# Performance work log

Hardware: AMD Instinct MI355X
Metric: run time of the kernel (lower is better)

Reference implementation:

```python
import jax, jax.numpy as jnp
import numpy as np

ALPHA = 1.0
EPS = 1e-7


def _giou_loss(pred, tgt):
    # pred, tgt: [..., 4] in (x1, y1, x2, y2); returns per-box loss 1 - GIoU
    px1, py1, px2, py2 = pred[..., 0], pred[..., 1], pred[..., 2], pred[..., 3]
    tx1, ty1, tx2, ty2 = tgt[..., 0], tgt[..., 1], tgt[..., 2], tgt[..., 3]
    area_p = (px2 - px1) * (py2 - py1)
    area_t = (tx2 - tx1) * (ty2 - ty1)
    iw = jnp.clip(jnp.minimum(px2, tx2) - jnp.maximum(px1, tx1), 0.0)
    ih = jnp.clip(jnp.minimum(py2, ty2) - jnp.maximum(py1, ty1), 0.0)
    inter = iw * ih
    union = area_p + area_t - inter
    iou = inter / (union + EPS)
    cw = jnp.maximum(px2, tx2) - jnp.minimum(px1, tx1)
    ch = jnp.maximum(py2, ty2) - jnp.minimum(py1, ty1)
    area_c = cw * ch
    giou = iou - (area_c - union) / (area_c + EPS)
    return 1.0 - giou


def _make_boxes(key, shape):
    k1, k2 = jax.random.split(key)
    xy1 = jax.random.uniform(k1, shape + (2,), jnp.float32) * 0.5
    wh = jax.random.uniform(k2, shape + (2,), jnp.float32) * 0.4 + 0.01
    return jnp.concatenate([xy1, xy1 + wh], axis=-1)


def setup_inputs() -> dict:
    key = jax.random.key(0)
    kc, kl, kt, kcls, kp = jax.random.split(key, 5)
    B, A, C = 64, 8732, 81
    confidences = jax.random.normal(kc, (B, A, C), jnp.float32)
    localizations = _make_boxes(kl, (B, A))
    tboxes = _make_boxes(kt, (B, A))
    is_pos = jax.random.uniform(kp, (B, A)) < 0.02
    cls = jnp.where(is_pos, jax.random.randint(kcls, (B, A), 1, C), 0)
    targets = jnp.concatenate([tboxes, cls[..., None].astype(jnp.float32)], axis=-1)
    return {"confidences": confidences, "localizations": localizations, "targets": targets}


def reference(confidences, localizations, targets):
    B, A, C = confidences.shape
    labels = targets[..., 4].astype(jnp.int32)     # [B, A]
    tboxes = targets[..., :4]                      # [B, A, 4]
    pos = labels > 0                               # [B, A]
    nm = pos.sum(axis=-1)                          # [B] num matched per item

    logp = jax.nn.log_softmax(confidences, axis=-1)          # [B, A, C]
    ce = -jnp.take_along_axis(logp, labels[..., None], axis=-1)[..., 0]  # CE vs label
    pos_loss = jnp.where(pos, ce, 0.0).sum(axis=-1)          # [B]

    # hard negative mining: CE vs background (class 0) on negatives only,
    # sort descending, keep top 3 * num_matched. CE >= 0, so mark positives
    # with -1 sentinel; they sort to the end and are excluded by (>= 0).
    neg_ce = jnp.where(pos, -1.0, -logp[..., 0])             # [B, A]
    sneg = -jnp.sort(-neg_ce, axis=-1)                       # descending
    ranks = jnp.arange(A)
    take = (ranks[None, :] < (3 * nm)[:, None]) & (sneg >= 0.0)
    neg_loss = jnp.where(take, sneg, 0.0).sum(axis=-1)       # [B]

    gl = _giou_loss(localizations, tboxes)                   # [B, A]
    loc_loss = jnp.where(pos, gl, 0.0).sum(axis=-1)          # [B]

    num_hits = nm.sum()
    total = (pos_loss + neg_loss + ALPHA * loc_loss).sum()
    denom = jnp.maximum(num_hits, 1).astype(total.dtype)
    has_hits = num_hits > 0
    loss = jnp.where(has_hits, total / denom, 0.0)
    conf_breakdown = jnp.where(has_hits, (pos_loss + neg_loss).sum() / denom, 0.0)
    loc_breakdown = jnp.where(has_hits, loc_loss.sum() / denom, 0.0)
    return loss, conf_breakdown, loc_breakdown
```

## Files before the change

### kernel.cpp

```cpp
#include <hip/hip_runtime.h>
#include <math.h>

#define NCLS 81
#define A_ANCH 8732
#define B_BATCH 64
#define NANCH (B_BATCH * A_ANCH)
#define EPSF 1e-7f

#define TILE 32
#define TDW  (TILE * NCLS)
#define BUFDW 2624
#define NT (NANCH / TILE)
#define GRID1 1792

static const size_t SBYTES = (size_t)NANCH * sizeof(float);

__global__ __launch_bounds__(64) void lse_kernel(
    const float* __restrict__ conf, float* __restrict__ sout,
    double* __restrict__ accum, unsigned long long* __restrict__ hits,
    unsigned int* __restrict__ done)
{
    __shared__ float sb[2][BUFDW];

    int tid = threadIdx.x;
    if (blockIdx.x == 0 && tid == 0) {
        accum[0] = 0.0; accum[1] = 0.0; *hits = 0ull; *done = 0u;
    }

    int a = tid & 31, h = tid >> 5;
    int t = blockIdx.x;

    float4 q0, q1, q2, q3, q4, q5, q6, q7, q8, q9;
    float qt = 0.f;

    {
        const float4* p = (const float4*)conf + (size_t)t * (TDW / 4);
        q0 = p[0 * 64 + tid]; q1 = p[1 * 64 + tid]; q2 = p[2 * 64 + tid];
        q3 = p[3 * 64 + tid]; q4 = p[4 * 64 + tid]; q5 = p[5 * 64 + tid];
        q6 = p[6 * 64 + tid]; q7 = p[7 * 64 + tid]; q8 = p[8 * 64 + tid];
        q9 = p[9 * 64 + tid];
        if (tid < 32) qt = conf[(size_t)t * TDW + 2560 + tid];
        float4* lp = (float4*)&sb[0][0];
        lp[0 * 64 + tid] = q0; lp[1 * 64 + tid] = q1; lp[2 * 64 + tid] = q2;
        lp[3 * 64 + tid] = q3; lp[4 * 64 + tid] = q4; lp[5 * 64 + tid] = q5;
        lp[6 * 64 + tid] = q6; lp[7 * 64 + tid] = q7; lp[8 * 64 + tid] = q8;
        lp[9 * 64 + tid] = q9;
        if (tid < 32) sb[0][2560 + tid] = qt;
    }
    int par = 0;

    #pragma clang loop unroll(disable)
    while (true) {
        int tn = t + GRID1;
        bool more = (tn < NT);
        if (more) {
            const float4* p = (const float4*)conf + (size_t)tn * (TDW / 4);
            q0 = p[0 * 64 + tid]; q1 = p[1 * 64 + tid]; q2 = p[2 * 64 + tid];
            q3 = p[3 * 64 + tid]; q4 = p[4 * 64 + tid]; q5 = p[5 * 64 + tid];
            q6 = p[6 * 64 + tid]; q7 = p[7 * 64 + tid]; q8 = p[8 * 64 + tid];
            q9 = p[9 * 64 + tid];
            if (tid < 32) qt = conf[(size_t)tn * TDW + 2560 + tid];
        }

        const float* r = &sb[par][a * 81 + h * 40];
        float x0 = r[0];
        float s0 = 0.f, s1 = 0.f, s2 = 0.f, s3 = 0.f;
        #pragma unroll
        for (int j = 0; j < 40; j += 4) {
            s0 += __expf(r[j]);
            s1 += __expf(r[j + 1]);
            s2 += __expf(r[j + 2]);
            s3 += __expf(r[j + 3]);
        }
        float s = (s0 + s1) + (s2 + s3) + (float)h * __expf(r[40]);
        s += __shfl_xor(s, 32);
        float res = __logf(s) - x0;

        if (!more) {
            if (h == 0) sout[(size_t)t * TILE + a] = res;
            break;
        }

        {
            float4* lp = (float4*)&sb[par ^ 1][0];
            lp[0 * 64 + tid] = q0; lp[1 * 64 + tid] = q1; lp[2 * 64 + tid] = q2;
            lp[3 * 64 + tid] = q3; lp[4 * 64 + tid] = q4; lp[5 * 64 + tid] = q5;
            lp[6 * 64 + tid] = q6; lp[7 * 64 + tid] = q7; lp[8 * 64 + tid] = q8;
            lp[9 * 64 + tid] = q9;
            if (tid < 32) sb[par ^ 1][2560 + tid] = qt;
        }
        if (h == 0) sout[(size_t)t * TILE + a] = res;

        t = tn; par ^= 1;
    }
}

#define K2_T 1024
#define VPT 9
#define NBIN 4096

__global__ __launch_bounds__(K2_T) void mine_kernel(
    const float* __restrict__ conf, const float* __restrict__ loc,
    const float* __restrict__ tgt, const float* __restrict__ sout,
    double* __restrict__ accum, unsigned long long* __restrict__ hits,
    unsigned int* __restrict__ done, float* __restrict__ out)
{
    __shared__ int   hist[NBIN];
    __shared__ int   wsum[16];
    __shared__ int   wex[16];
    __shared__ int   selB, selCab;
    __shared__ float fs[4];
    __shared__ int   c0_s, cg_s, nm_s;

    int b = blockIdx.x, tid = threadIdx.x;
    int lane = tid & 63, wid = tid >> 6;

    for (int i = tid; i < NBIN; i += K2_T) hist[i] = 0;
    if (tid < 4)  fs[tid] = 0.f;
    if (tid == 0) { c0_s = 0; cg_s = 0; nm_s = 0; }
    __syncthreads();

    float v[VPT]; int lab[VPT];
    size_t base = (size_t)b * A_ANCH;
    #pragma unroll
    for (int i = 0; i < VPT; ++i) {
        int idx = tid + i * K2_T;
        bool in = idx < A_ANCH;
        v[i]   = in ? sout[base + idx] : -1.f;
        lab[i] = in ? (int)tgt[(base + idx) * 5 + 4] : 0;
    }

    float pce = 0.f, ploc = 0.f; int pc = 0;
    #pragma unroll
    for (int i = 0; i < VPT; ++i) {
        if (lab[i] > 0) {
            size_t gi = base + (size_t)(tid + i * K2_T);
            float r0 = conf[gi * NCLS];
            float rl = conf[gi * NCLS + lab[i]];
            pce += v[i] + r0 - rl;
            float4 p = *(const float4*)(loc + gi * 4);
            const float* tg = tgt + gi * 5;
            float tx1 = tg[0], ty1 = tg[1], tx2 = tg[2], ty2 = tg[3];
            float area_p = (p.z - p.x) * (p.w - p.y);
            float area_t = (tx2 - tx1) * (ty2 - ty1);
            float iw = fmaxf(fminf(p.z, tx2) - fmaxf(p.x, tx1), 0.f);
            float ih = fmaxf(fminf(p.w, ty2) - fmaxf(p.y, ty1), 0.f);
            float inter = iw * ih;
            float uni   = area_p + area_t - inter;
            float iou   = inter / (uni + EPSF);
            float cw = fmaxf(p.z, tx2) - fminf(p.x, tx1);
            float ch = fmaxf(p.w, ty2) - fminf(p.y, ty1);
            float area_c = cw * ch;
            ploc += 1.f - (iou - (area_c - uni) / (area_c + EPSF));
            pc++;
            v[i] = -1.f;
        }
    }
    int c = 0; float sa = 0.f;
    #pragma unroll
    for (int i = 0; i < VPT; ++i) { if (v[i] >= 0.f) { c++; sa += v[i]; } }
    for (int off = 32; off; off >>= 1) {
        pc += __shfl_xor(pc, off);  pce += __shfl_xor(pce, off);
        ploc += __shfl_xor(ploc, off);
        c  += __shfl_xor(c, off);   sa  += __shfl_xor(sa, off);
    }
    if (lane == 0) {
        if (pc) atomicAdd(&nm_s, pc);
        atomicAdd(&fs[2], pce);
        atomicAdd(&fs[3], ploc);
        atomicAdd(&c0_s, c);
        atomicAdd(&fs[0], sa);
    }
    __syncthreads();

    int k = 3 * nm_s;
    int c0 = c0_s; float sall = fs[0];
    float negl = 0.f;

    if (k > 0) {
        if (k >= c0) {
            negl = sall;
        } else {
            int B1v = 0, B2v = 0, kk = k;
            for (int lvl = 0; lvl < 2; ++lvl) {
                if (lvl == 1) {
                    for (int i = tid; i < NBIN; i += K2_T) hist[i] = 0;
                    __syncthreads();
                }
                #pragma unroll
                for (int i = 0; i < VPT; ++i) {
                    if (v[i] >= 0.f) {
                        unsigned bits = __float_as_uint(v[i]);
                        if (lvl == 0) {
                            atomicAdd(&hist[bits >> 19], 1);
                        } else if ((int)(bits >> 19) == B1v) {
                            atomicAdd(&hist[(bits >> 7) & 4095], 1);
                        }
                    }
                }
                __syncthreads();

                int b0 = tid * 4;
                int h0 = hist[b0], h1 = hist[b0 + 1], h2 = hist[b0 + 2], h3 = hist[b0 + 3];
                int tsum = h0 + h1 + h2 + h3;
                int ssum = tsum;
                #pragma unroll
                for (int off = 1; off < 64; off <<= 1) {
                    int o = __shfl_down(ssum, off);
                    ssum += (lane + off < 64) ? o : 0;
                }
                if (lane == 0) wsum[wid] = ssum;
                __syncthreads();
                if (wid == 0) {
                    int wv = (lane < 16) ? wsum[lane] : 0;
                    int ws = wv;
                    #pragma unroll
                    for (int off = 1; off < 64; off <<= 1) {
                        int o = __shfl_down(ws, off);
                        ws += (lane + off < 64) ? o : 0;
                    }
                    if (lane < 16) wex[lane] = ws - wv;
                }
                __syncthreads();
                int above = wex[wid] + (ssum - tsum);
                if (above < kk && above + tsum >= kk) {
                    int cum = above, B = b0;
                    if      (cum + h3 >= kk) { B = b0 + 3; }
                    else if (cum + h3 + h2 >= kk) { cum += h3; B = b0 + 2; }
                    else if (cum + h3 + h2 + h1 >= kk) { cum += h3 + h2; B = b0 + 1; }
                    else { cum += h3 + h2 + h1; B = b0; }
                    selB = B; selCab = cum;
                }
                __syncthreads();
                if (lvl == 0) { B1v = selB; } else { B2v = selB; }
                kk -= selCab;
                __syncthreads();
            }

            unsigned tk = ((unsigned)B1v << 12) | (unsigned)B2v;
            float tval = __uint_as_float(((unsigned)B1v << 19) | ((unsigned)B2v << 7));
            int cg = 0; float sg = 0.f;
            #pragma unroll
            for (int i = 0; i < VPT; ++i) {
                if (v[i] >= 0.f) {
                    unsigned key = __float_as_uint(v[i]) >> 7;
                    if (key > tk) { cg++; sg += v[i]; }
                }
            }
            for (int off = 32; off; off >>= 1) {
                cg += __shfl_xor(cg, off); sg += __shfl_xor(sg, off);
            }
            if (lane == 0) { atomicAdd(&cg_s, cg); atomicAdd(&fs[1], sg); }
            __syncthreads();
            negl = fs[1] + (float)(k - cg_s) * tval;
        }
    }

    if (tid == 0) {
        atomicAdd(&accum[0], (double)(fs[2] + negl));
        atomicAdd(&accum[1], (double)fs[3]);
        atomicAdd(hits, (unsigned long long)nm_s);
        __threadfence();
        unsigned old = atomicAdd(done, 1u);
        if (old == B_BATCH - 1) {
            double conf_s = __hip_atomic_load(&accum[0], __ATOMIC_ACQUIRE, __HIP_MEMORY_SCOPE_AGENT);
            double loc_s  = __hip_atomic_load(&accum[1], __ATOMIC_ACQUIRE, __HIP_MEMORY_SCOPE_AGENT);
            unsigned long long h = __hip_atomic_load(hits, __ATOMIC_ACQUIRE, __HIP_MEMORY_SCOPE_AGENT);
            double denom = (double)(h > 0 ? h : 1ull);
            if (h > 0) {
                out[0] = (float)((conf_s + loc_s) / denom);
                out[1] = (float)(conf_s / denom);
                out[2] = (float)(loc_s / denom);
            } else {
                out[0] = 0.f; out[1] = 0.f; out[2] = 0.f;
            }
        }
    }
}

extern "C" void kernel_launch(void* const* d_in, const int* in_sizes, int n_in,
                              void* d_out, int out_size, void* d_ws, size_t ws_size,
                              hipStream_t stream) {
    const float* conf = (const float*)d_in[0];
    const float* loc  = (const float*)d_in[1];
    const float* tgt  = (const float*)d_in[2];
    float* out = (float*)d_out;

    char* ws = (char*)d_ws;
    float* sout = (float*)ws;
    double* accum = (double*)(ws + SBYTES);
    unsigned long long* hits = (unsigned long long*)(ws + SBYTES + 16);
    unsigned int* done = (unsigned int*)(ws + SBYTES + 24);

    lse_kernel<<<dim3(GRID1), dim3(64), 0, stream>>>(conf, sout, accum, hits, done);
    mine_kernel<<<dim3(B_BATCH), dim3(K2_T), 0, stream>>>(
        conf, loc, tgt, sout, accum, hits, done, out);
}
```

Before: 50.18 us.

## Compute per-anchor logsumexp from registers without shared-memory staging

The LSE kernel drops the double-buffered shared-memory tile and instead has each group of 8 lanes load float4 pieces of 4 anchors' rows straight from global memory. Each lane accumulates exponentials into per-anchor partial sums, using compile-time boundary handling for float4s that straddle two rows, then reduces with xor shuffles. The aim is to remove the LDS write/read traffic and barriers, and to raise occupancy with 256-thread blocks and more waves. The cost is the loss of the explicit load/compute overlap across tiles, plus extra select logic and shuffles in each group.

```diff
diff --git a/kernel.cpp b/kernel.cpp
--- a/kernel.cpp
+++ b/kernel.cpp
@@ -7,91 +7,78 @@
 #define NANCH (B_BATCH * A_ANCH)
 #define EPSF 1e-7f
 
-#define TILE 32
-#define TDW  (TILE * NCLS)
-#define BUFDW 2624
-#define NT (NANCH / TILE)
-#define GRID1 1792
+#define GROUPS (NANCH / 32)
+#define LBLK 256
+#define LGRID 2183
+#define NWAVE (LGRID * 4)
 
 static const size_t SBYTES = (size_t)NANCH * sizeof(float);
 
-__global__ __launch_bounds__(64) void lse_kernel(
+#define ACC_ADD(KK, val) do {            \
+    if      ((KK) == 0) a0 += (val);     \
+    else if ((KK) == 1) a1 += (val);     \
+    else if ((KK) == 2) a2 += (val);     \
+    else                a3 += (val);     \
+} while (0)
+
+#define PROC(r, c, comp) do {                              \
+    const int lo = 32 * (r) + (c);                         \
+    const int K  = lo / 81;                                \
+    const int K2 = (lo + 28) / 81;                         \
+    float ev = __expf(comp);                               \
+    if (K == K2) { ACC_ADD(K, ev); }                       \
+    else {                                                 \
+        const int T = (81 * (K + 1) - lo + 3) / 4;         \
+        float hv = (j >= T) ? ev : 0.f;                    \
+        ACC_ADD(K, ev - hv); ACC_ADD(K + 1, hv);           \
+    }                                                      \
+} while (0)
+
+#define PROCQ(r, qv) do {        \
+    PROC(r, 0, (qv).x);          \
+    PROC(r, 1, (qv).y);          \
+    PROC(r, 2, (qv).z);          \
+    PROC(r, 3, (qv).w);          \
+} while (0)
+
+__global__ __launch_bounds__(LBLK) void lse_kernel(
     const float* __restrict__ conf, float* __restrict__ sout,
     double* __restrict__ accum, unsigned long long* __restrict__ hits,
     unsigned int* __restrict__ done)
 {
-    __shared__ float sb[2][BUFDW];
-
     int tid = threadIdx.x;
     if (blockIdx.x == 0 && tid == 0) {
         accum[0] = 0.0; accum[1] = 0.0; *hits = 0ull; *done = 0u;
     }
-
-    int a = tid & 31, h = tid >> 5;
-    int t = blockIdx.x;
-
-    float4 q0, q1, q2, q3, q4, q5, q6, q7, q8, q9;
-    float qt = 0.f;
-
-    {
-        const float4* p = (const float4*)conf + (size_t)t * (TDW / 4);
-        q0 = p[0 * 64 + tid]; q1 = p[1 * 64 + tid]; q2 = p[2 * 64 + tid];
-        q3 = p[3 * 64 + tid]; q4 = p[4 * 64 + tid]; q5 = p[5 * 64 + tid];
-        q6 = p[6 * 64 + tid]; q7 = p[7 * 64 + tid]; q8 = p[8 * 64 + tid];
-        q9 = p[9 * 64 + tid];
-        if (tid < 32) qt = conf[(size_t)t * TDW + 2560 + tid];
-        float4* lp = (float4*)&sb[0][0];
-        lp[0 * 64 + tid] = q0; lp[1 * 64 + tid] = q1; lp[2 * 64 + tid] = q2;
-        lp[3 * 64 + tid] = q3; lp[4 * 64 + tid] = q4; lp[5 * 64 + tid] = q5;
-        lp[6 * 64 + tid] = q6; lp[7 * 64 + tid] = q7; lp[8 * 64 + tid] = q8;
-        lp[9 * 64 + tid] = q9;
-        if (tid < 32) sb[0][2560 + tid] = qt;
-    }
-    int par = 0;
+    int w = blockIdx.x * 4 + (tid >> 6);
+    int lane = tid & 63;
+    int o = lane >> 3, j = lane & 7;
 
     #pragma clang loop unroll(disable)
-    while (true) {
-        int tn = t + GRID1;
-        bool more = (tn < NT);
-        if (more) {
-            const float4* p = (const float4*)conf + (size_t)tn * (TDW / 4);
-            q0 = p[0 * 64 + tid]; q1 = p[1 * 64 + tid]; q2 = p[2 * 64 + tid];
-            q3 = p[3 * 64 + tid]; q4 = p[4 * 64 + tid]; q5 = p[5 * 64 + tid];
-            q6 = p[6 * 64 + tid]; q7 = p[7 * 64 + tid]; q8 = p[8 * 64 + tid];
-            q9 = p[9 * 64 + tid];
-            if (tid < 32) qt = conf[(size_t)tn * TDW + 2560 + tid];
-        }
-
-        const float* r = &sb[par][a * 81 + h * 40];
-        float x0 = r[0];
-        float s0 = 0.f, s1 = 0.f, s2 = 0.f, s3 = 0.f;
+    for (int g = w; g < GROUPS; g += NWAVE) {
+        const float4* p = (const float4*)conf + (size_t)g * 648 + o * 81 + j;
+        float4 q0 = p[0],  q1 = p[8],  q2 = p[16], q3 = p[24], q4 = p[32];
+        float4 q5 = p[40], q6 = p[48], q7 = p[56], q8 = p[64], q9 = p[72];
+        float4 q10 = make_float4(-INFINITY, -INFINITY, -INFINITY, -INFINITY);
+        if (j == 0) q10 = p[80];
+        float x0 = 0.f;
+        if (j < 4) x0 = conf[(size_t)g * 2592 + (o * 4 + j) * 81];
+
+        float a0 = 0.f, a1 = 0.f, a2 = 0.f, a3 = 0.f;
+        PROCQ(0, q0); PROCQ(1, q1); PROCQ(2, q2); PROCQ(3, q3); PROCQ(4, q4);
+        PROCQ(5, q5); PROCQ(6, q6); PROCQ(7, q7); PROCQ(8, q8); PROCQ(9, q9);
+        a3 += __expf(q10.x); a3 += __expf(q10.y);
+        a3 += __expf(q10.z); a3 += __expf(q10.w);
+
         #pragma unroll
-        for (int j = 0; j < 40; j += 4) {
-            s0 += __expf(r[j]);
-            s1 += __expf(r[j + 1]);
-            s2 += __expf(r[j + 2]);
-            s3 += __expf(r[j + 3]);
-        }
-        float s = (s0 + s1) + (s2 + s3) + (float)h * __expf(r[40]);
-        s += __shfl_xor(s, 32);
-        float res = __logf(s) - x0;
-
-        if (!more) {
-            if (h == 0) sout[(size_t)t * TILE + a] = res;
-            break;
-        }
-
-        {
-            float4* lp = (float4*)&sb[par ^ 1][0];
-            lp[0 * 64 + tid] = q0; lp[1 * 64 + tid] = q1; lp[2 * 64 + tid] = q2;
-            lp[3 * 64 + tid] = q3; lp[4 * 64 + tid] = q4; lp[5 * 64 + tid] = q5;
-            lp[6 * 64 + tid] = q6; lp[7 * 64 + tid] = q7; lp[8 * 64 + tid] = q8;
-            lp[9 * 64 + tid] = q9;
-            if (tid < 32) sb[par ^ 1][2560 + tid] = qt;
-        }
-        if (h == 0) sout[(size_t)t * TILE + a] = res;
-
-        t = tn; par ^= 1;
+        for (int d = 1; d < 8; d <<= 1) {
+            a0 += __shfl_xor(a0, d); a1 += __shfl_xor(a1, d);
+            a2 += __shfl_xor(a2, d); a3 += __shfl_xor(a3, d);
+        }
+        if (j < 4) {
+            float m = (j == 0) ? a0 : (j == 1) ? a1 : (j == 2) ? a2 : a3;
+            sout[(size_t)g * 32 + o * 4 + j] = __logf(m) - x0;
+        }
     }
 }
 
@@ -206,8 +193,8 @@
                 int ssum = tsum;
                 #pragma unroll
                 for (int off = 1; off < 64; off <<= 1) {
-                    int o = __shfl_down(ssum, off);
-                    ssum += (lane + off < 64) ? o : 0;
+                    int oo = __shfl_down(ssum, off);
+                    ssum += (lane + off < 64) ? oo : 0;
                 }
                 if (lane == 0) wsum[wid] = ssum;
                 __syncthreads();
@@ -216,8 +203,8 @@
                     int ws = wv;
                     #pragma unroll
                     for (int off = 1; off < 64; off <<= 1) {
-                        int o = __shfl_down(ws, off);
-                        ws += (lane + off < 64) ? o : 0;
+                        int oo = __shfl_down(ws, off);
+                        ws += (lane + off < 64) ? oo : 0;
                     }
                     if (lane < 16) wex[lane] = ws - wv;
                 }
@@ -292,7 +279,7 @@
     unsigned long long* hits = (unsigned long long*)(ws + SBYTES + 16);
     unsigned int* done = (unsigned int*)(ws + SBYTES + 24);
 
-    lse_kernel<<<dim3(GRID1), dim3(64), 0, stream>>>(conf, sout, accum, hits, done);
+    lse_kernel<<<dim3(LGRID), dim3(LBLK), 0, stream>>>(conf, sout, accum, hits, done);
     mine_kernel<<<dim3(B_BATCH), dim3(K2_T), 0, stream>>>(
         conf, loc, tgt, sout, accum, hits, done, out);
 }
```

Measured after the change: 50.15 us. No clear change (-0.1%).
